# Kernel optimization log

Hardware: AMD Instinct MI355X
Metric: run time of the kernel (lower is better)

Reference implementation:

```python
import jax, jax.numpy as jnp
import numpy as np
import math

D_MODEL = 512
N_HEADS = 16
HEAD_DIM = D_MODEL // N_HEADS  # 32
ROPE_BASE = 10000.0
B, T = 2, 2048


def build_rope_cache(seq_len, dim, base):
    inv_freq = 1.0 / (base ** (jnp.arange(0, dim, 2, dtype=jnp.float32) / dim))  # (dim/2,)
    t = jnp.arange(seq_len, dtype=jnp.float32)
    freqs = jnp.outer(t, inv_freq)                  # (T, dim/2)
    emb = jnp.concatenate([freqs, freqs], axis=-1)  # (T, dim)
    return jnp.cos(emb), jnp.sin(emb)


def rotate_half(x):
    x1, x2 = jnp.split(x, 2, axis=-1)
    return jnp.concatenate([-x2, x1], axis=-1)


def apply_rope(x, cos, sin):
    # x: (B,H,T,hd); cos/sin: (T,hd) broadcast over B,H
    return x * cos + rotate_half(x) * sin


def setup_inputs() -> dict:
    key = jax.random.key(0)
    k1, k2, k3 = jax.random.split(key, 3)
    x = jax.random.normal(k1, (B, T, D_MODEL), dtype=jnp.float32)
    w_qkv = jax.random.normal(k2, (3 * D_MODEL, D_MODEL), dtype=jnp.float32) * 0.02
    w_o = jax.random.normal(k3, (D_MODEL, D_MODEL), dtype=jnp.float32) * 0.02
    return {"x": x, "w_qkv": w_qkv, "w_o": w_o}


def reference(x, w_qkv, w_o):
    Bx, Tx, C = x.shape
    H, hd = N_HEADS, HEAD_DIM
    qkv = x @ w_qkv.T                                   # (B,T,3C)
    qkv = qkv.reshape(Bx, Tx, 3, H, hd).transpose(0, 2, 3, 1, 4)  # (B,3,H,T,hd)
    q, k, v = qkv[:, 0], qkv[:, 1], qkv[:, 2]
    cos, sin = build_rope_cache(Tx, hd, ROPE_BASE)
    q = apply_rope(q, cos, sin)
    k = apply_rope(k, cos, sin)
    scale = 1.0 / math.sqrt(hd)
    scores = jnp.einsum('bhqd,bhkd->bhqk', q, k) * scale  # (B,H,T,T)
    causal = jnp.tril(jnp.ones((Tx, Tx), dtype=bool))
    scores = jnp.where(causal, scores, jnp.finfo(scores.dtype).min)
    attn = jax.nn.softmax(scores, axis=-1)
    out = jnp.einsum('bhqk,bhkd->bhqd', attn, v)          # (B,H,T,hd)
    out = out.transpose(0, 2, 1, 3).reshape(Bx, Tx, C)    # (B,T,C)
    return out @ w_o.T
```

## Files before the change

### kernel.cpp

```cpp
#include <hip/hip_runtime.h>
#include <hip/hip_bf16.h>
#include <math.h>

#define D_MODEL 512
#define N_HEADS 16
#define HEAD_DIM 32
#define T_SEQ 2048
#define B_SZ 2
#define NTOK (B_SZ * T_SEQ)
#define QKV_DIM (3 * D_MODEL)

typedef short short8 __attribute__((ext_vector_type(8)));
typedef float f32x4  __attribute__((ext_vector_type(4)));

__device__ __forceinline__ float bf2f(unsigned int u16) {
    union { unsigned int i; float f; } v;
    v.i = u16 << 16;
    return v.f;
}

__device__ __forceinline__ unsigned short f2bf(float f) {
    union { float f; unsigned int i; } v;
    v.f = f;
    unsigned int lsb = (v.i >> 16) & 1u;
    v.i += 0x7fffu + lsb;
    return (unsigned short)(v.i >> 16);
}

__device__ __forceinline__ void gld_lds16(const void* g, void* l) {
    __builtin_amdgcn_global_load_lds(
        (const __attribute__((address_space(1))) void*)g,
        (__attribute__((address_space(3))) void*)l, 16, 0, 0);
}

#define N4_X   (NTOK * D_MODEL / 4)
#define N4_WQ  (QKV_DIM * D_MODEL / 4)
#define N4_WO  (D_MODEL * D_MODEL / 4)
__global__ __launch_bounds__(256) void cvt_all(const float* __restrict__ x,
                                               const float* __restrict__ wq,
                                               const float* __restrict__ wo,
                                               unsigned short* __restrict__ xb,
                                               unsigned short* __restrict__ wqb,
                                               unsigned short* __restrict__ wob) {
    int i = blockIdx.x * 256 + threadIdx.x;
    const float* in;
    unsigned short* out;
    int k;
    if (i < N4_X)                { in = x;  out = xb;  k = i; }
    else if (i < N4_X + N4_WQ)   { in = wq; out = wqb; k = i - N4_X; }
    else if (i < N4_X + N4_WQ + N4_WO) { in = wo; out = wob; k = i - N4_X - N4_WQ; }
    else return;
    float4 v = ((const float4*)in)[k];
    ushort4 o;
    o.x = f2bf(v.x); o.y = f2bf(v.y); o.z = f2bf(v.z); o.w = f2bf(v.w);
    ((ushort4*)out)[k] = o;
}

#define LOG2_10000_D16 0.8304820237218405f

template<int LDA, int LDC, bool OUT_BF16, bool ROPE>
__global__ __launch_bounds__(256) void gemm_nt64(const unsigned short* __restrict__ A,
                                                 const unsigned short* __restrict__ B,
                                                 void* __restrict__ Cout) {
    __shared__ unsigned short Als[64 * 64];
    __shared__ unsigned short Bls[64 * 64];

    const int tid = threadIdx.x;
    const int m0 = blockIdx.y * 64;
    const int n0 = blockIdx.x * 64;

    const int wid  = tid >> 6;
    const int lane = tid & 63;
    const int c    = lane & 15;
    const int quad = lane >> 4;
    const int wm = (wid >> 1) * 32;
    const int wn = (wid & 1) * 32;

    f32x4 acc[2][2];
#pragma unroll
    for (int i = 0; i < 2; ++i)
#pragma unroll
        for (int j = 0; j < 2; ++j) acc[i][j] = (f32x4)0.f;

    const int srow = wid * 8 + (lane >> 3);
    const int schk = lane & 7;

    for (int k0 = 0; k0 < 512; k0 += 64) {
#pragma unroll
        for (int it = 0; it < 2; ++it) {
            const unsigned short* g = A + (size_t)(m0 + it * 32 + srow) * LDA + k0 + schk * 8;
            gld_lds16(g, &Als[(it * 32 + srow) * 64 + schk * 8]);
        }
#pragma unroll
        for (int it = 0; it < 2; ++it) {
            const unsigned short* g = B + (size_t)(n0 + it * 32 + srow) * 512 + k0 + schk * 8;
            gld_lds16(g, &Bls[(it * 32 + srow) * 64 + schk * 8]);
        }
        __syncthreads();

#pragma unroll
        for (int kk = 0; kk < 2; ++kk) {
            short8 af[2], bfr[2];
#pragma unroll
            for (int i = 0; i < 2; ++i)
                af[i] = *(const short8*)&Als[(wm + i * 16 + c) * 64 + kk * 32 + quad * 8];
#pragma unroll
            for (int j = 0; j < 2; ++j)
                bfr[j] = *(const short8*)&Bls[(wn + j * 16 + c) * 64 + kk * 32 + quad * 8];
#pragma unroll
            for (int i = 0; i < 2; ++i)
#pragma unroll
                for (int j = 0; j < 2; ++j)
                    acc[i][j] = __builtin_amdgcn_mfma_f32_16x16x32_bf16(af[i], bfr[j], acc[i][j], 0, 0, 0);
        }
        __syncthreads();
    }

    if (ROPE) {
        const int sec = n0 >> 9;
        if (sec < 2) {
            const float invf = exp2f(-LOG2_10000_D16 * (float)c);
            const float sc = (sec == 0) ? 0.17677669529663687f : 1.0f;
#pragma unroll
            for (int i = 0; i < 2; ++i)
#pragma unroll
                for (int r = 0; r < 4; ++r) {
                    int t = (m0 + wm + i * 16 + quad * 4 + r) & (T_SEQ - 1);
                    float ss, cc;
                    sincosf((float)t * invf, &ss, &cc);
                    float e0 = acc[i][0][r], e1 = acc[i][1][r];
                    acc[i][0][r] = (e0 * cc - e1 * ss) * sc;
                    acc[i][1][r] = (e1 * cc + e0 * ss) * sc;
                }
        }
    }

    if (OUT_BF16) {
        unsigned short* Cb = (unsigned short*)Cout;
#pragma unroll
        for (int i = 0; i < 2; ++i)
#pragma unroll
            for (int j = 0; j < 2; ++j)
#pragma unroll
                for (int r = 0; r < 4; ++r) {
                    int mm = m0 + wm + i * 16 + quad * 4 + r;
                    int nn = n0 + wn + j * 16 + c;
                    Cb[(size_t)mm * LDC + nn] = f2bf(acc[i][j][r]);
                }
    } else {
        float* Cf = (float*)Cout;
#pragma unroll
        for (int i = 0; i < 2; ++i)
#pragma unroll
            for (int j = 0; j < 2; ++j)
#pragma unroll
                for (int r = 0; r < 4; ++r) {
                    int mm = m0 + wm + i * 16 + quad * 4 + r;
                    int nn = n0 + wn + j * 16 + c;
                    Cf[(size_t)mm * LDC + nn] = acc[i][j][r];
                }
    }
}

#define PSTR 72

__global__ __launch_bounds__(256) void flash_attn(unsigned short* __restrict__ qkv) {
    __shared__ unsigned short Kt[64 * 32];
    __shared__ unsigned short VtT[32 * PSTR];
    __shared__ unsigned short Pl[4 * 16 * PSTR];

    const int qtile = (gridDim.x - 1) - blockIdx.x;
    const int bh    = blockIdx.y;
    const int b = bh >> 4, h = bh & 15;
    const int tid  = threadIdx.x;
    const int wid  = tid >> 6;
    const int lane = tid & 63;
    const int c    = lane & 15;
    const int quad = lane >> 4;

    const int q0w = qtile * 64 + wid * 16;
    const size_t rowbase = (size_t)(b * T_SEQ) * QKV_DIM;

    short8 qf = *(const short8*)(qkv + rowbase + (size_t)(q0w + c) * QKV_DIM + h * HEAD_DIM + quad * 8);

    f32x4 accO[2];
    accO[0] = (f32x4)0.f; accO[1] = (f32x4)0.f;
    float l_r[4] = {0.f, 0.f, 0.f, 0.f};

    const int srow = tid >> 2;
    const int sch  = tid & 3;

    int vswz[2];
#pragma unroll
    for (int ns = 0; ns < 2; ++ns) {
        int d = ns * 16 + c;
        vswz[ns] = (d & 7) ^ ((d >> 3) << 1);
    }

    const int nkt = qtile + 1;
    for (int kt = 0; kt < nkt; ++kt) {
        {
            const size_t krow = rowbase + (size_t)(kt * 64 + srow) * QKV_DIM + h * HEAD_DIM + sch * 8;
            gld_lds16(qkv + krow + D_MODEL, &Kt[tid * 8]);
            uint4 v = *(const uint4*)(qkv + krow + 2 * D_MODEL);
            unsigned short hv[8];
            hv[0] = v.x & 0xffffu; hv[1] = v.x >> 16;
            hv[2] = v.y & 0xffffu; hv[3] = v.y >> 16;
            hv[4] = v.z & 0xffffu; hv[5] = v.z >> 16;
            hv[6] = v.w & 0xffffu; hv[7] = v.w >> 16;
            const int kblk = srow >> 3, kin = srow & 7, schx = sch << 1;
#pragma unroll
            for (int i = 0; i < 8; ++i) {
                int d   = sch * 8 + i;
                int blk = kblk ^ i ^ schx;
                VtT[d * PSTR + blk * 8 + kin] = hv[i];
            }
        }
        __syncthreads();

        f32x4 sv[4];
#pragma unroll
        for (int j = 0; j < 4; ++j) {
            short8 kf = *(const short8*)&Kt[(j * 16 + c) * 32 + quad * 8];
            f32x4 z = (f32x4)0.f;
            sv[j] = __builtin_amdgcn_mfma_f32_16x16x32_bf16(qf, kf, z, 0, 0, 0);
        }

        if (kt == qtile) {
#pragma unroll
            for (int j = 0; j < 4; ++j)
#pragma unroll
                for (int r = 0; r < 4; ++r)
                    if (j * 16 + c > wid * 16 + quad * 4 + r) sv[j][r] = -30000.f;
        }

        unsigned short* plw = &Pl[wid * 16 * PSTR];
#pragma unroll
        for (int j = 0; j < 4; ++j)
#pragma unroll
            for (int r = 0; r < 4; ++r) {
                float p = __expf(sv[j][r]);
                l_r[r] += p;
                plw[(quad * 4 + r) * PSTR + j * 16 + c] = f2bf(p);
            }

#pragma unroll
        for (int kk = 0; kk < 2; ++kk) {
            short8 pf = *(const short8*)&plw[c * PSTR + kk * 32 + quad * 8];
#pragma unroll
            for (int ns = 0; ns < 2; ++ns) {
                int d   = ns * 16 + c;
                int blk = (kk * 4 + quad) ^ vswz[ns];
                short8 vf = *(const short8*)&VtT[d * PSTR + blk * 8];
                accO[ns] = __builtin_amdgcn_mfma_f32_16x16x32_bf16(pf, vf, accO[ns], 0, 0, 0);
            }
        }
        __syncthreads();
    }

#pragma unroll
    for (int r = 0; r < 4; ++r) {
        float lr = l_r[r];
        lr += __shfl_xor(lr, 1);
        lr += __shfl_xor(lr, 2);
        lr += __shfl_xor(lr, 4);
        lr += __shfl_xor(lr, 8);
        float inv = 1.f / lr;
        int qg = q0w + quad * 4 + r;
        unsigned short* op = qkv + rowbase + (size_t)qg * QKV_DIM + h * HEAD_DIM;
#pragma unroll
        for (int ns = 0; ns < 2; ++ns)
            op[ns * 16 + c] = f2bf(accO[ns][r] * inv);
    }
}

extern "C" void kernel_launch(void* const* d_in, const int* in_sizes, int n_in,
                              void* d_out, int out_size, void* d_ws, size_t ws_size,
                              hipStream_t stream) {
    const float* x     = (const float*)d_in[0];
    const float* w_qkv = (const float*)d_in[1];
    const float* w_o   = (const float*)d_in[2];
    float* out = (float*)d_out;

    unsigned short* qkv = (unsigned short*)d_ws;
    unsigned short* xb  = qkv + (size_t)NTOK * QKV_DIM;
    unsigned short* wqb = xb  + (size_t)NTOK * D_MODEL;
    unsigned short* wob = wqb + (size_t)QKV_DIM * D_MODEL;

    {
        int total = N4_X + N4_WQ + N4_WO;
        cvt_all<<<(total + 255) / 256, 256, 0, stream>>>(x, w_qkv, w_o, xb, wqb, wob);
    }
    {
        dim3 grid(QKV_DIM / 64, NTOK / 64);
        gemm_nt64<D_MODEL, QKV_DIM, true, true><<<grid, 256, 0, stream>>>(xb, wqb, qkv);
    }
    {
        dim3 grid(T_SEQ / 64, B_SZ * N_HEADS);
        flash_attn<<<grid, 256, 0, stream>>>(qkv);
    }
    {
        dim3 grid(D_MODEL / 64, NTOK / 64);
        gemm_nt64<QKV_DIM, D_MODEL, false, false><<<grid, 256, 0, stream>>>(qkv, wob, out);
    }
}
```

Measured before the change: 142.8 us.

## Write V transposed from QKV GEMM and run per-wave attention without LDS staging

The QKV GEMM epilogue now writes V into a separate transposed buffer, and its M tile grows to 128. Flash attention is reorganised so each wave handles an independent 16-row query block across 1024 blocks. It reads K and transposed V directly from global memory, which removes LDS staging and the __syncthreads barriers. The Q scale is folded into a log2 factor so the kernel can use exp2f, and P is truncated to bf16 instead of rounded. This trades shared-memory reuse for more global/L2 traffic, and truncation adds a slight precision loss.

```diff
diff --git a/kernel.cpp b/kernel.cpp
--- a/kernel.cpp
+++ b/kernel.cpp
@@ -24,6 +24,12 @@
     v.f = f;
     unsigned int lsb = (v.i >> 16) & 1u;
     v.i += 0x7fffu + lsb;
+    return (unsigned short)(v.i >> 16);
+}
+
+__device__ __forceinline__ unsigned short f2bf_trunc(float f) {
+    union { float f; unsigned int i; } v;
+    v.f = f;
     return (unsigned short)(v.i >> 16);
 }
 
@@ -57,28 +63,31 @@
 }
 
 #define LOG2_10000_D16 0.8304820237218405f
-
-template<int LDA, int LDC, bool OUT_BF16, bool ROPE>
-__global__ __launch_bounds__(256) void gemm_nt64(const unsigned short* __restrict__ A,
-                                                 const unsigned short* __restrict__ B,
-                                                 void* __restrict__ Cout) {
-    __shared__ unsigned short Als[64 * 64];
+#define QSCALE_LOG2 0.2550348788f
+
+template<int MT, int LDA, int LDC, bool OUT_BF16, bool ROPE>
+__global__ __launch_bounds__(256) void gemm_nt(const unsigned short* __restrict__ A,
+                                               const unsigned short* __restrict__ B,
+                                               void* __restrict__ Cout,
+                                               unsigned short* __restrict__ vt) {
+    __shared__ unsigned short Als[MT * 64];
     __shared__ unsigned short Bls[64 * 64];
 
     const int tid = threadIdx.x;
-    const int m0 = blockIdx.y * 64;
+    const int m0 = blockIdx.y * MT;
     const int n0 = blockIdx.x * 64;
 
     const int wid  = tid >> 6;
     const int lane = tid & 63;
     const int c    = lane & 15;
     const int quad = lane >> 4;
-    const int wm = (wid >> 1) * 32;
+    const int wm = (wid >> 1) * (MT / 2);
     const int wn = (wid & 1) * 32;
-
-    f32x4 acc[2][2];
-#pragma unroll
-    for (int i = 0; i < 2; ++i)
+    const int MI = MT / 32;
+
+    f32x4 acc[MI][2];
+#pragma unroll
+    for (int i = 0; i < MI; ++i)
 #pragma unroll
         for (int j = 0; j < 2; ++j) acc[i][j] = (f32x4)0.f;
 
@@ -87,7 +96,7 @@
 
     for (int k0 = 0; k0 < 512; k0 += 64) {
 #pragma unroll
-        for (int it = 0; it < 2; ++it) {
+        for (int it = 0; it < MT / 32; ++it) {
             const unsigned short* g = A + (size_t)(m0 + it * 32 + srow) * LDA + k0 + schk * 8;
             gld_lds16(g, &Als[(it * 32 + srow) * 64 + schk * 8]);
         }
@@ -100,15 +109,15 @@
 
 #pragma unroll
         for (int kk = 0; kk < 2; ++kk) {
-            short8 af[2], bfr[2];
-#pragma unroll
-            for (int i = 0; i < 2; ++i)
+            short8 af[MI], bfr[2];
+#pragma unroll
+            for (int i = 0; i < MI; ++i)
                 af[i] = *(const short8*)&Als[(wm + i * 16 + c) * 64 + kk * 32 + quad * 8];
 #pragma unroll
             for (int j = 0; j < 2; ++j)
                 bfr[j] = *(const short8*)&Bls[(wn + j * 16 + c) * 64 + kk * 32 + quad * 8];
 #pragma unroll
-            for (int i = 0; i < 2; ++i)
+            for (int i = 0; i < MI; ++i)
 #pragma unroll
                 for (int j = 0; j < 2; ++j)
                     acc[i][j] = __builtin_amdgcn_mfma_f32_16x16x32_bf16(af[i], bfr[j], acc[i][j], 0, 0, 0);
@@ -120,9 +129,9 @@
         const int sec = n0 >> 9;
         if (sec < 2) {
             const float invf = exp2f(-LOG2_10000_D16 * (float)c);
-            const float sc = (sec == 0) ? 0.17677669529663687f : 1.0f;
-#pragma unroll
-            for (int i = 0; i < 2; ++i)
+            const float sc = (sec == 0) ? QSCALE_LOG2 : 1.0f;
+#pragma unroll
+            for (int i = 0; i < MI; ++i)
 #pragma unroll
                 for (int r = 0; r < 4; ++r) {
                     int t = (m0 + wm + i * 16 + quad * 4 + r) & (T_SEQ - 1);
@@ -132,13 +141,30 @@
                     acc[i][0][r] = (e0 * cc - e1 * ss) * sc;
                     acc[i][1][r] = (e1 * cc + e0 * ss) * sc;
                 }
+        } else {
+            unsigned short* Vt = vt;
+#pragma unroll
+            for (int i = 0; i < MI; ++i)
+#pragma unroll
+                for (int j = 0; j < 2; ++j) {
+                    int nl = n0 - 2 * D_MODEL + wn + j * 16;
+                    int head = nl >> 5;
+                    int d = (nl & 16) + c;
+                    int t = m0 + wm + i * 16 + quad * 4;
+                    int bI = t >> 11;
+                    ushort4 st;
+                    st.x = f2bf(acc[i][j][0]); st.y = f2bf(acc[i][j][1]);
+                    st.z = f2bf(acc[i][j][2]); st.w = f2bf(acc[i][j][3]);
+                    *(ushort4*)(Vt + ((size_t)((bI * 16 + head) * 32 + d)) * 2048 + (t & 2047)) = st;
+                }
+            return;
         }
     }
 
     if (OUT_BF16) {
         unsigned short* Cb = (unsigned short*)Cout;
 #pragma unroll
-        for (int i = 0; i < 2; ++i)
+        for (int i = 0; i < MI; ++i)
 #pragma unroll
             for (int j = 0; j < 2; ++j)
 #pragma unroll
@@ -150,7 +176,7 @@
     } else {
         float* Cf = (float*)Cout;
 #pragma unroll
-        for (int i = 0; i < 2; ++i)
+        for (int i = 0; i < MI; ++i)
 #pragma unroll
             for (int j = 0; j < 2; ++j)
 #pragma unroll
@@ -164,84 +190,61 @@
 
 #define PSTR 72
 
-__global__ __launch_bounds__(256) void flash_attn(unsigned short* __restrict__ qkv) {
-    __shared__ unsigned short Kt[64 * 32];
-    __shared__ unsigned short VtT[32 * PSTR];
+__global__ __launch_bounds__(256) void flash_attn(unsigned short* __restrict__ qkv,
+                                                  const unsigned short* __restrict__ vt) {
     __shared__ unsigned short Pl[4 * 16 * PSTR];
 
-    const int qtile = (gridDim.x - 1) - blockIdx.x;
-    const int bh    = blockIdx.y;
-    const int b = bh >> 4, h = bh & 15;
     const int tid  = threadIdx.x;
     const int wid  = tid >> 6;
     const int lane = tid & 63;
     const int c    = lane & 15;
     const int quad = lane >> 4;
 
-    const int q0w = qtile * 64 + wid * 16;
+    const int w  = blockIdx.x * 4 + wid;
+    const int g  = 127 - (w >> 5);
+    const int bh = w & 31;
+    const int b = bh >> 4, h = bh & 15;
+
+    const int qr = g * 16;
     const size_t rowbase = (size_t)(b * T_SEQ) * QKV_DIM;
 
-    short8 qf = *(const short8*)(qkv + rowbase + (size_t)(q0w + c) * QKV_DIM + h * HEAD_DIM + quad * 8);
+    short8 qf = *(const short8*)(qkv + rowbase + (size_t)(qr + c) * QKV_DIM + h * HEAD_DIM + quad * 8);
 
     f32x4 accO[2];
     accO[0] = (f32x4)0.f; accO[1] = (f32x4)0.f;
     float l_r[4] = {0.f, 0.f, 0.f, 0.f};
 
-    const int srow = tid >> 2;
-    const int sch  = tid & 3;
-
-    int vswz[2];
-#pragma unroll
-    for (int ns = 0; ns < 2; ++ns) {
-        int d = ns * 16 + c;
-        vswz[ns] = (d & 7) ^ ((d >> 3) << 1);
-    }
-
-    const int nkt = qtile + 1;
+    const int nkt = (g >> 2) + 1;
+    const int qo  = (g & 3) * 16;
+    unsigned short* plw = &Pl[wid * 16 * PSTR];
+
+    const unsigned short* kp = qkv + rowbase + D_MODEL + h * HEAD_DIM + quad * 8;
+    const unsigned short* vp = vt + (size_t)(bh * 32) * 2048 + quad * 8;
+
     for (int kt = 0; kt < nkt; ++kt) {
-        {
-            const size_t krow = rowbase + (size_t)(kt * 64 + srow) * QKV_DIM + h * HEAD_DIM + sch * 8;
-            gld_lds16(qkv + krow + D_MODEL, &Kt[tid * 8]);
-            uint4 v = *(const uint4*)(qkv + krow + 2 * D_MODEL);
-            unsigned short hv[8];
-            hv[0] = v.x & 0xffffu; hv[1] = v.x >> 16;
-            hv[2] = v.y & 0xffffu; hv[3] = v.y >> 16;
-            hv[4] = v.z & 0xffffu; hv[5] = v.z >> 16;
-            hv[6] = v.w & 0xffffu; hv[7] = v.w >> 16;
-            const int kblk = srow >> 3, kin = srow & 7, schx = sch << 1;
-#pragma unroll
-            for (int i = 0; i < 8; ++i) {
-                int d   = sch * 8 + i;
-                int blk = kblk ^ i ^ schx;
-                VtT[d * PSTR + blk * 8 + kin] = hv[i];
-            }
-        }
-        __syncthreads();
-
         f32x4 sv[4];
 #pragma unroll
         for (int j = 0; j < 4; ++j) {
-            short8 kf = *(const short8*)&Kt[(j * 16 + c) * 32 + quad * 8];
+            short8 kf = *(const short8*)(kp + (size_t)(kt * 64 + j * 16 + c) * QKV_DIM);
             f32x4 z = (f32x4)0.f;
             sv[j] = __builtin_amdgcn_mfma_f32_16x16x32_bf16(qf, kf, z, 0, 0, 0);
         }
 
-        if (kt == qtile) {
+        if (kt == nkt - 1) {
 #pragma unroll
             for (int j = 0; j < 4; ++j)
 #pragma unroll
                 for (int r = 0; r < 4; ++r)
-                    if (j * 16 + c > wid * 16 + quad * 4 + r) sv[j][r] = -30000.f;
-        }
-
-        unsigned short* plw = &Pl[wid * 16 * PSTR];
+                    if (j * 16 + c > qo + quad * 4 + r) sv[j][r] = -30000.f;
+        }
+
 #pragma unroll
         for (int j = 0; j < 4; ++j)
 #pragma unroll
             for (int r = 0; r < 4; ++r) {
-                float p = __expf(sv[j][r]);
+                float p = exp2f(sv[j][r]);
                 l_r[r] += p;
-                plw[(quad * 4 + r) * PSTR + j * 16 + c] = f2bf(p);
+                plw[(quad * 4 + r) * PSTR + j * 16 + c] = f2bf_trunc(p);
             }
 
 #pragma unroll
@@ -249,13 +252,10 @@
             short8 pf = *(const short8*)&plw[c * PSTR + kk * 32 + quad * 8];
 #pragma unroll
             for (int ns = 0; ns < 2; ++ns) {
-                int d   = ns * 16 + c;
-                int blk = (kk * 4 + quad) ^ vswz[ns];
-                short8 vf = *(const short8*)&VtT[d * PSTR + blk * 8];
+                short8 vf = *(const short8*)(vp + (size_t)(ns * 16 + c) * 2048 + kt * 64 + kk * 32);
                 accO[ns] = __builtin_amdgcn_mfma_f32_16x16x32_bf16(pf, vf, accO[ns], 0, 0, 0);
             }
         }
-        __syncthreads();
     }
 
 #pragma unroll
@@ -266,7 +266,7 @@
         lr += __shfl_xor(lr, 4);
         lr += __shfl_xor(lr, 8);
         float inv = 1.f / lr;
-        int qg = q0w + quad * 4 + r;
+        int qg = qr + quad * 4 + r;
         unsigned short* op = qkv + rowbase + (size_t)qg * QKV_DIM + h * HEAD_DIM;
 #pragma unroll
         for (int ns = 0; ns < 2; ++ns)
@@ -286,21 +286,21 @@
     unsigned short* xb  = qkv + (size_t)NTOK * QKV_DIM;
     unsigned short* wqb = xb  + (size_t)NTOK * D_MODEL;
     unsigned short* wob = wqb + (size_t)QKV_DIM * D_MODEL;
+    unsigned short* vt  = wob + (size_t)D_MODEL * D_MODEL;
 
     {
         int total = N4_X + N4_WQ + N4_WO;
         cvt_all<<<(total + 255) / 256, 256, 0, stream>>>(x, w_qkv, w_o, xb, wqb, wob);
     }
     {
-        dim3 grid(QKV_DIM / 64, NTOK / 64);
-        gemm_nt64<D_MODEL, QKV_DIM, true, true><<<grid, 256, 0, stream>>>(xb, wqb, qkv);
+        dim3 grid(QKV_DIM / 64, NTOK / 128);
+        gemm_nt<128, D_MODEL, QKV_DIM, true, true><<<grid, 256, 0, stream>>>(xb, wqb, qkv, vt);
     }
     {
-        dim3 grid(T_SEQ / 64, B_SZ * N_HEADS);
-        flash_attn<<<grid, 256, 0, stream>>>(qkv);
+        flash_attn<<<1024, 256, 0, stream>>>(qkv, vt);
     }
     {
         dim3 grid(D_MODEL / 64, NTOK / 64);
-        gemm_nt64<QKV_DIM, D_MODEL, false, false><<<grid, 256, 0, stream>>>(qkv, wob, out);
-    }
-}
+        gemm_nt<64, QKV_DIM, D_MODEL, false, false><<<grid, 256, 0, stream>>>(qkv, wob, out, nullptr);
+    }
+}
```

New measurement: 163.2 us. +14.3%, slower.
